# Performance work log

Hardware: AMD Instinct MI355X
Metric: run time of the kernel (lower is better)

## Reference

```python
import jax, jax.numpy as jnp
import numpy as np

# Distilled RGBDVideoTower.forward 'voxelize' pooling path:
#   p2v = voxelize(feat_xyz, voxel_size)  (per-batch compacted voxel ids)
#   pooled = cat([scatter_mean(video_features[b], p2v[b]) for b in range(B)])
#   batch_offset = cumsum(num_voxels_per_batch)
# Static-shape JAX version: each batch's pooled output is padded to K slots
# (empty voxel slots are zero); batch_offset holds the true per-batch counts.

B, N, F = 8, 9216, 1024          # scenes, patch tokens per scene (16 views * 24*24), CLIP-L dim
K = 4096                          # static cap on voxels per scene (xyz in [0,3.2)^3, voxel 0.2 -> 16^3)
VOXEL_SIZE = 0.2
XYZ_SCALE = 3.2
HASH_M = 1024                     # per-axis hash multiplier (coords << 1024)


def setup_inputs() -> dict:
    key = jax.random.key(0)
    k1, k2 = jax.random.split(key)
    features = jax.random.normal(k1, (B, N, F), dtype=jnp.float32)
    xyz = jax.random.uniform(k2, (B, N, 3), dtype=jnp.float32) * XYZ_SCALE
    return {"features": features, "xyz": xyz}


def _pool_one(feat, ids):
    """feat: (N, F), ids: (N,) int32 voxel hash -> (K, F) mean-pooled, count."""
    order = jnp.argsort(ids)
    s = ids[order]
    # mark start of each run of equal voxel ids -> compacted voxel index (rank)
    new_seg = jnp.concatenate([jnp.ones((1,), jnp.int32),
                               (s[1:] != s[:-1]).astype(jnp.int32)])
    rank = jnp.cumsum(new_seg) - 1            # (N,) 0..count-1 in sorted order
    count = rank[-1] + 1                       # number of occupied voxels
    seg = jnp.zeros_like(ids).at[order].set(rank)  # back to original point order
    sums = jax.ops.segment_sum(feat, seg, num_segments=K)            # (K, F)
    cnt = jax.ops.segment_sum(jnp.ones((feat.shape[0],), feat.dtype), seg,
                              num_segments=K)                         # (K,)
    pooled = sums / jnp.maximum(cnt, 1.0)[:, None]  # scatter_mean; empty slots stay 0
    return pooled, count


def reference(features, xyz):
    coords = jnp.floor(xyz / VOXEL_SIZE).astype(jnp.int32)        # (B, N, 3)
    coords = coords - coords.min(axis=1, keepdims=True)           # nonneg per batch
    ids = (coords[..., 0] * HASH_M + coords[..., 1]) * HASH_M + coords[..., 2]
    pooled, counts = jax.vmap(_pool_one)(features, ids)           # (B, K, F), (B,)
    batch_offset = jnp.cumsum(counts).astype(jnp.int32)           # (B,)
    return pooled.reshape(B * K, F), batch_offset
```

## Files before the change

### kernel.cpp

```cpp
#include <hip/hip_runtime.h>
#include <math.h>

#define BB 8
#define NN 9216
#define FF 1024
#define KK 4096
#define VOX 0.2f


__global__ __launch_bounds__(256) void k_hist(const float* __restrict__ xyz,
                                              int* __restrict__ keys,
                                              int* __restrict__ cnt) {
    int p = blockIdx.x * 256 + threadIdx.x;
    if (p >= BB * NN) return;
    int b = p / NN;
    const float* x = xyz + (size_t)p * 3;
    int c0 = (int)floorf(x[0] / VOX);
    int c1 = (int)floorf(x[1] / VOX);
    int c2 = (int)floorf(x[2] / VOX);
    c0 = min(max(c0, 0), 15);
    c1 = min(max(c1, 0), 15);
    c2 = min(max(c2, 0), 15);
    int key = (c0 << 8) | (c1 << 4) | c2;
    keys[p] = key;
    atomicAdd(&cnt[b * KK + key], 1);
}

__global__ __launch_bounds__(1024) void k_scan(const int* __restrict__ cnt,
                                               int* __restrict__ start,
                                               int2* __restrict__ rank_info,
                                               int* __restrict__ counts) {
    const int b = blockIdx.x;
    const int t = threadIdx.x;
    __shared__ unsigned long long s_scan[1024];
    const int base = t * 4;
    int c[4];
    int to = 0, tc = 0;
    for (int j = 0; j < 4; j++) {
        c[j] = cnt[b * KK + base + j];
        to += (c[j] > 0);
        tc += c[j];
    }
    unsigned long long v = ((unsigned long long)(unsigned)to << 32) | (unsigned)tc;
    s_scan[t] = v;
    __syncthreads();
    for (int off = 1; off < 1024; off <<= 1) {
        unsigned long long add = (t >= off) ? s_scan[t - off] : 0ULL;
        __syncthreads();
        s_scan[t] += add;
        __syncthreads();
    }
    unsigned long long incl = s_scan[t];
    unsigned long long excl = incl - v;
    int rank = (int)(excl >> 32);
    int st   = (int)(excl & 0xffffffffULL);
    for (int j = 0; j < 4; j++) {
        start[b * KK + base + j] = st;
        if (c[j] > 0) {
            rank_info[b * KK + rank] = make_int2(st, c[j]);
            rank++;
        }
        st += c[j];
    }
    if (t == 1023) counts[b] = (int)(incl >> 32);
}

__global__ __launch_bounds__(256) void k_order(const int* __restrict__ keys,
                                               const int* __restrict__ start,
                                               int* __restrict__ cursor,
                                               int* __restrict__ order,
                                               const int* __restrict__ counts,
                                               float* __restrict__ out_off) {
    int p = blockIdx.x * 256 + threadIdx.x;
    if (p == 0) {
        int cum = 0;
        for (int b = 0; b < BB; b++) {
            cum += counts[b];
            out_off[b] = (float)cum;
        }
    }
    if (p >= BB * NN) return;
    int b = p / NN;
    int lp = p - b * NN;
    int key = keys[p];
    int pos = atomicAdd(&cursor[b * KK + key], 1);
    order[(size_t)b * NN + start[b * KK + key] + pos] = lp;
}

__global__ __launch_bounds__(256) void k_pool(const float* __restrict__ feat,
                                              const int2* __restrict__ rank_info,
                                              const int* __restrict__ order,
                                              const int* __restrict__ counts,
                                              float* __restrict__ out) {
    const int blk = blockIdx.x;
    const int b = blk >> 12;
    const int k = blk & (KK - 1);
    const int t = threadIdx.x;
    float4 a0 = make_float4(0.f, 0.f, 0.f, 0.f);
    float4 a1 = make_float4(0.f, 0.f, 0.f, 0.f);
    if (k < counts[b]) {
        int2 info = rank_info[(size_t)b * KK + k];
        const int s = info.x, c = info.y;
        const float* fb = feat + (size_t)b * NN * FF;
        const int* ob = order + (size_t)b * NN + s;
        int i = 0;
        for (; i + 1 < c; i += 2) {
            int p0 = ob[i], p1 = ob[i + 1];
            float4 v0 = ((const float4*)(fb + (size_t)p0 * FF))[t];
            float4 v1 = ((const float4*)(fb + (size_t)p1 * FF))[t];
            a0.x += v0.x; a0.y += v0.y; a0.z += v0.z; a0.w += v0.w;
            a1.x += v1.x; a1.y += v1.y; a1.z += v1.z; a1.w += v1.w;
        }
        if (i < c) {
            int p0 = ob[i];
            float4 v0 = ((const float4*)(fb + (size_t)p0 * FF))[t];
            a0.x += v0.x; a0.y += v0.y; a0.z += v0.z; a0.w += v0.w;
        }
        float fc = (float)c;
        a0.x = (a0.x + a1.x) / fc;
        a0.y = (a0.y + a1.y) / fc;
        a0.z = (a0.z + a1.z) / fc;
        a0.w = (a0.w + a1.w) / fc;
    }
    ((float4*)(out + (size_t)blk * FF))[t] = a0;
}

extern "C" void kernel_launch(void* const* d_in, const int* in_sizes, int n_in,
                              void* d_out, int out_size, void* d_ws, size_t ws_size,
                              hipStream_t stream) {
    const float* features = (const float*)d_in[0];
    const float* xyz      = (const float*)d_in[1];
    float* out = (float*)d_out;

    int* ws        = (int*)d_ws;
    int* cnt       = ws;
    int* cursor    = cnt    + BB * KK;
    int* keys      = cursor + BB * KK;
    int* start     = keys   + BB * NN;
    int2* rankinfo = (int2*)(start + BB * KK);
    int* counts    = (int*)(rankinfo + BB * KK);
    int* order     = counts + BB;

    hipMemsetAsync(cnt, 0, 2 * BB * KK * sizeof(int), stream);
    k_hist<<<(BB * NN + 255) / 256, 256, 0, stream>>>(xyz, keys, cnt);
    k_scan<<<BB, 1024, 0, stream>>>(cnt, start, rankinfo, counts);
    k_order<<<(BB * NN + 255) / 256, 256, 0, stream>>>(keys, start, cursor, order,
                                                       counts, out + (size_t)BB * KK * FF);
    k_pool<<<BB * KK, 256, 0, stream>>>(features, rankinfo, order, counts, out);
}
```

Baseline: 447.9 us.

## Pack slot position into keys, use wave-shuffle scan, nontemporal loads/stores in pool

The histogram kernel now stores the atomic return value packed with the voxel key, so the order kernel no longer needs a second cursor array with its own atomics and memset. The scan kernel replaces the shared-memory Hillis-Steele scan and its many barriers with a wave-level shuffle scan plus a small cross-wave step, and uses vectorised int4 loads and stores. The pool kernel switches to ext_vector float4 arithmetic and nontemporal loads and stores for the feature stream and output. Most of the time is in the bandwidth-bound pool kernel, so the cheaper small kernels may matter little, and the nontemporal hints could change cache behaviour when several voxels share a row.

Result: faster. 420.1 us (-6.2%).

```diff
diff --git a/kernel.cpp b/kernel.cpp
--- a/kernel.cpp
+++ b/kernel.cpp
@@ -6,6 +6,8 @@
 #define FF 1024
 #define KK 4096
 #define VOX 0.2f
+
+typedef float f32x4 __attribute__((ext_vector_type(4)));
 
 
 __global__ __launch_bounds__(256) void k_hist(const float* __restrict__ xyz,
@@ -22,8 +24,8 @@
     c1 = min(max(c1, 0), 15);
     c2 = min(max(c2, 0), 15);
     int key = (c0 << 8) | (c1 << 4) | c2;
-    keys[p] = key;
-    atomicAdd(&cnt[b * KK + key], 1);
+    int pos = atomicAdd(&cnt[b * KK + key], 1);
+    keys[p] = (key << 14) | pos;
 }
 
 __global__ __launch_bounds__(1024) void k_scan(const int* __restrict__ cnt,
@@ -32,42 +34,58 @@
                                                int* __restrict__ counts) {
     const int b = blockIdx.x;
     const int t = threadIdx.x;
-    __shared__ unsigned long long s_scan[1024];
-    const int base = t * 4;
-    int c[4];
+    const int lane = t & 63;
+    const int wv = t >> 6;
+    __shared__ unsigned long long s_wave[16];
+
+    int4 c4 = ((const int4*)(cnt + b * KK))[t];
+    int c[4] = {c4.x, c4.y, c4.z, c4.w};
     int to = 0, tc = 0;
-    for (int j = 0; j < 4; j++) {
-        c[j] = cnt[b * KK + base + j];
-        to += (c[j] > 0);
-        tc += c[j];
+    #pragma unroll
+    for (int j = 0; j < 4; j++) { to += (c[j] > 0); tc += c[j]; }
+    unsigned long long v = ((unsigned long long)(unsigned)to << 32) | (unsigned)tc;
+
+    unsigned long long x = v;
+    #pragma unroll
+    for (int off = 1; off < 64; off <<= 1) {
+        unsigned long long y = __shfl_up(x, off, 64);
+        if (lane >= off) x += y;
     }
-    unsigned long long v = ((unsigned long long)(unsigned)to << 32) | (unsigned)tc;
-    s_scan[t] = v;
+    if (lane == 63) s_wave[wv] = x;
     __syncthreads();
-    for (int off = 1; off < 1024; off <<= 1) {
-        unsigned long long add = (t >= off) ? s_scan[t - off] : 0ULL;
-        __syncthreads();
-        s_scan[t] += add;
-        __syncthreads();
+    if (wv == 0) {
+        unsigned long long w = (lane < 16) ? s_wave[lane] : 0ULL;
+        #pragma unroll
+        for (int off = 1; off < 16; off <<= 1) {
+            unsigned long long y = __shfl_up(w, off, 64);
+            if (lane >= off) w += y;
+        }
+        if (lane < 16) s_wave[lane] = w;
     }
-    unsigned long long incl = s_scan[t];
+    __syncthreads();
+
+    unsigned long long incl = x + (wv ? s_wave[wv - 1] : 0ULL);
     unsigned long long excl = incl - v;
     int rank = (int)(excl >> 32);
     int st   = (int)(excl & 0xffffffffULL);
+    int4 s4;
+    int sts[4];
+    #pragma unroll
     for (int j = 0; j < 4; j++) {
-        start[b * KK + base + j] = st;
+        sts[j] = st;
         if (c[j] > 0) {
-            rank_info[b * KK + rank] = make_int2(st, c[j]);
+            rank_info[(size_t)b * KK + rank] = make_int2(st, c[j]);
             rank++;
         }
         st += c[j];
     }
+    s4.x = sts[0]; s4.y = sts[1]; s4.z = sts[2]; s4.w = sts[3];
+    ((int4*)(start + b * KK))[t] = s4;
     if (t == 1023) counts[b] = (int)(incl >> 32);
 }
 
 __global__ __launch_bounds__(256) void k_order(const int* __restrict__ keys,
                                                const int* __restrict__ start,
-                                               int* __restrict__ cursor,
                                                int* __restrict__ order,
                                                const int* __restrict__ counts,
                                                float* __restrict__ out_off) {
@@ -82,8 +100,9 @@
     if (p >= BB * NN) return;
     int b = p / NN;
     int lp = p - b * NN;
-    int key = keys[p];
-    int pos = atomicAdd(&cursor[b * KK + key], 1);
+    int packed = keys[p];
+    int key = packed >> 14;
+    int pos = packed & 0x3fff;
     order[(size_t)b * NN + start[b * KK + key] + pos] = lp;
 }
 
@@ -96,8 +115,8 @@
     const int b = blk >> 12;
     const int k = blk & (KK - 1);
     const int t = threadIdx.x;
-    float4 a0 = make_float4(0.f, 0.f, 0.f, 0.f);
-    float4 a1 = make_float4(0.f, 0.f, 0.f, 0.f);
+    f32x4 a0 = {0.f, 0.f, 0.f, 0.f};
+    f32x4 a1 = {0.f, 0.f, 0.f, 0.f};
     if (k < counts[b]) {
         int2 info = rank_info[(size_t)b * KK + k];
         const int s = info.x, c = info.y;
@@ -106,23 +125,17 @@
         int i = 0;
         for (; i + 1 < c; i += 2) {
             int p0 = ob[i], p1 = ob[i + 1];
-            float4 v0 = ((const float4*)(fb + (size_t)p0 * FF))[t];
-            float4 v1 = ((const float4*)(fb + (size_t)p1 * FF))[t];
-            a0.x += v0.x; a0.y += v0.y; a0.z += v0.z; a0.w += v0.w;
-            a1.x += v1.x; a1.y += v1.y; a1.z += v1.z; a1.w += v1.w;
+            f32x4 v0 = __builtin_nontemporal_load((const f32x4*)(fb + (size_t)p0 * FF) + t);
+            f32x4 v1 = __builtin_nontemporal_load((const f32x4*)(fb + (size_t)p1 * FF) + t);
+            a0 += v0; a1 += v1;
         }
         if (i < c) {
             int p0 = ob[i];
-            float4 v0 = ((const float4*)(fb + (size_t)p0 * FF))[t];
-            a0.x += v0.x; a0.y += v0.y; a0.z += v0.z; a0.w += v0.w;
+            a0 += __builtin_nontemporal_load((const f32x4*)(fb + (size_t)p0 * FF) + t);
         }
-        float fc = (float)c;
-        a0.x = (a0.x + a1.x) / fc;
-        a0.y = (a0.y + a1.y) / fc;
-        a0.z = (a0.z + a1.z) / fc;
-        a0.w = (a0.w + a1.w) / fc;
+        a0 = (a0 + a1) / (float)c;
     }
-    ((float4*)(out + (size_t)blk * FF))[t] = a0;
+    __builtin_nontemporal_store(a0, (f32x4*)(out + (size_t)blk * FF) + t);
 }
 
 extern "C" void kernel_launch(void* const* d_in, const int* in_sizes, int n_in,
@@ -134,17 +147,16 @@
 
     int* ws        = (int*)d_ws;
     int* cnt       = ws;
-    int* cursor    = cnt    + BB * KK;
-    int* keys      = cursor + BB * KK;
+    int* keys      = cnt    + BB * KK;
     int* start     = keys   + BB * NN;
     int2* rankinfo = (int2*)(start + BB * KK);
     int* counts    = (int*)(rankinfo + BB * KK);
     int* order     = counts + BB;
 
-    hipMemsetAsync(cnt, 0, 2 * BB * KK * sizeof(int), stream);
+    hipMemsetAsync(cnt, 0, BB * KK * sizeof(int), stream);
     k_hist<<<(BB * NN + 255) / 256, 256, 0, stream>>>(xyz, keys, cnt);
     k_scan<<<BB, 1024, 0, stream>>>(cnt, start, rankinfo, counts);
-    k_order<<<(BB * NN + 255) / 256, 256, 0, stream>>>(keys, start, cursor, order,
-                                                       counts, out + (size_t)BB * KK * FF);
+    k_order<<<(BB * NN + 255) / 256, 256, 0, stream>>>(keys, start, order, counts,
+                                                       out + (size_t)BB * KK * FF);
     k_pool<<<BB * KK, 256, 0, stream>>>(features, rankinfo, order, counts, out);
 }
```
